# Optimization experiments

Measured on AMD Instinct MI355X. Metric: run time of the kernel, lower is better.

The kernel has to match this reference:

```python
import jax, jax.numpy as jnp
import numpy as np

N_NODES = 50000
N_EDGES = 800000
IN_DIM = 768
HID = 256
OUT = 9
EDGE_FEAT = 100
N_TYPES = 50
N_DIST = 128
P_DROP = 0.4


def _argcn_conv(x, src, dst, etype, edist, W_msg, W_root, b, type_emb, dist_emb, gate_w, gate_b, n_nodes):
    """Edge-type/distance gated relational graph conv.
    x: [N, in]; src/dst/etype/edist: [E]; returns [N, out].
    """
    # per-edge feature from type + distance embeddings -> scalar gate
    ef = jnp.concatenate([type_emb[etype], dist_emb[edist]], axis=-1)  # [E, 2*EDGE_FEAT]
    alpha = jax.nn.sigmoid(ef @ gate_w + gate_b)                       # [E, 1]
    # transform at nodes first (N x in x out GEMM), then gather per edge
    xt = x @ W_msg                                                     # [N, out]
    msg = alpha * xt[src]                                              # [E, out]
    agg = jax.ops.segment_sum(msg, dst, num_segments=n_nodes)         # [N, out]
    return agg + x @ W_root + b


def setup_inputs() -> dict:
    key = jax.random.key(0)
    ks = jax.random.split(key, 20)
    s_in = 1.0 / np.sqrt(IN_DIM)
    s_hid = 1.0 / np.sqrt(HID)
    s_ef = 1.0 / np.sqrt(2 * EDGE_FEAT)
    inp = {
        "x": jax.random.normal(ks[0], (N_NODES, IN_DIM), dtype=jnp.float32),
        "edge_index": jax.random.randint(ks[1], (2, N_EDGES), 0, N_NODES, dtype=jnp.int64 if jax.config.jax_enable_x64 else jnp.int32),
        "edge_type": jax.random.randint(ks[2], (N_EDGES,), 0, N_TYPES, dtype=jnp.int32),
        "edge_distance": jax.random.randint(ks[3], (N_EDGES,), 0, N_DIST, dtype=jnp.int32),
        "drop1": jax.random.uniform(ks[4], (N_NODES, HID), dtype=jnp.float32),
        "drop2": jax.random.uniform(ks[5], (N_NODES, OUT), dtype=jnp.float32),
        # conv1 params
        "W1_msg": jax.random.normal(ks[6], (IN_DIM, HID), dtype=jnp.float32) * s_in,
        "W1_root": jax.random.normal(ks[7], (IN_DIM, HID), dtype=jnp.float32) * s_in,
        "b1": jnp.zeros((HID,), dtype=jnp.float32),
        "te1": jax.random.normal(ks[8], (N_TYPES, EDGE_FEAT), dtype=jnp.float32) * 0.02,
        "de1": jax.random.normal(ks[9], (N_DIST, EDGE_FEAT), dtype=jnp.float32) * 0.02,
        "g1_w": jax.random.normal(ks[10], (2 * EDGE_FEAT, 1), dtype=jnp.float32) * s_ef,
        "g1_b": jnp.zeros((1,), dtype=jnp.float32),
        # conv2 params
        "W2_msg": jax.random.normal(ks[11], (HID, OUT), dtype=jnp.float32) * s_hid,
        "W2_root": jax.random.normal(ks[12], (HID, OUT), dtype=jnp.float32) * s_hid,
        "b2": jnp.zeros((OUT,), dtype=jnp.float32),
        "te2": jax.random.normal(ks[13], (N_TYPES, EDGE_FEAT), dtype=jnp.float32) * 0.02,
        "de2": jax.random.normal(ks[14], (N_DIST, EDGE_FEAT), dtype=jnp.float32) * 0.02,
        "g2_w": jax.random.normal(ks[15], (2 * EDGE_FEAT, 1), dtype=jnp.float32) * s_ef,
        "g2_b": jnp.zeros((1,), dtype=jnp.float32),
    }
    return inp


def reference(x, edge_index, edge_type, edge_distance, drop1, drop2,
              W1_msg, W1_root, b1, te1, de1, g1_w, g1_b,
              W2_msg, W2_root, b2, te2, de2, g2_w, g2_b):
    src, dst = edge_index[0], edge_index[1]
    n = x.shape[0]
    inv_keep = 1.0 / (1.0 - P_DROP)
    m1 = (drop1 >= P_DROP).astype(x.dtype) * inv_keep  # inverted dropout mask
    m2 = (drop2 >= P_DROP).astype(x.dtype) * inv_keep

    h = _argcn_conv(x, src, dst, edge_type, edge_distance,
                    W1_msg, W1_root, b1, te1, de1, g1_w, g1_b, n)
    h = jax.nn.relu(h * m1)
    h = _argcn_conv(h, src, dst, edge_type, edge_distance,
                    W2_msg, W2_root, b2, te2, de2, g2_w, g2_b, n)
    h = jax.nn.relu(h * m2)
    return h
```

## Files before the change

kernel.cpp:

```cpp
#include <hip/hip_runtime.h>
#include <math.h>

#define N_NODES   50000
#define N_EDGESC  800000
#define IN_DIM    768
#define HID       256
#define OUT_DIM   9
#define EDGE_FEAT 100
#define P_DROP    0.4f
#define INV_KEEP  (1.0f/0.6f)

typedef __attribute__((ext_vector_type(8))) short bf16x8;
typedef __attribute__((ext_vector_type(4))) float f32x4;

__device__ __forceinline__ ushort f2bf(float f) {
    uint u = __float_as_uint(f);
    uint r = (u + 0x7fffu + ((u >> 16) & 1u)) >> 16;
    return (ushort)r;
}
__device__ __forceinline__ float bf2f(ushort h) {
    return __uint_as_float(((uint)h) << 16);
}

__device__ __forceinline__ int swz1(int row, int byte) { return byte ^ (((row >> 1) & 3) << 4); }
__device__ __forceinline__ int swz2(int row, int byte) { return byte ^ ((row & 7) << 4); }

__global__ void gate_tables(const float* __restrict__ te1, const float* __restrict__ de1,
                            const float* __restrict__ g1w,
                            const float* __restrict__ te2, const float* __restrict__ de2,
                            const float* __restrict__ g2w,
                            float* __restrict__ tbl) {
    int t = threadIdx.x;
    const float* vec; const float* w;
    if (t < 50)       { vec = te1 + t*EDGE_FEAT;         w = g1w; }
    else if (t < 178) { vec = de1 + (t-50)*EDGE_FEAT;    w = g1w + EDGE_FEAT; }
    else if (t < 228) { vec = te2 + (t-178)*EDGE_FEAT;   w = g2w; }
    else if (t < 356) { vec = de2 + (t-228)*EDGE_FEAT;   w = g2w + EDGE_FEAT; }
    else return;
    float s = 0.f;
    for (int i = 0; i < EDGE_FEAT; ++i) s += vec[i]*w[i];
    tbl[t] = s;
}

__global__ __launch_bounds__(256) void bt_prep(const float* __restrict__ Wm, const float* __restrict__ Wr,
                                               ushort* __restrict__ BTh, ushort* __restrict__ BTl) {
    int tid = blockIdx.x*256 + threadIdx.x;
    if (tid >= 512*IN_DIM) return;
    int n = tid / IN_DIM, k = tid % IN_DIM;
    float w = (n < HID) ? Wm[(size_t)k*HID + n] : Wr[(size_t)k*HID + (n - HID)];
    ushort hi = f2bf(w);
    BTh[tid] = hi;
    BTl[tid] = f2bf(w - bf2f(hi));
}

__global__ __launch_bounds__(256) void w2_pack(const float* __restrict__ Wm, const float* __restrict__ Wr,
                                               ushort* __restrict__ WPT) {
    int i = blockIdx.x*256 + threadIdx.x;
    if (i >= 32*256) return;
    int col = i >> 8, k = i & 255;
    float v = 0.f;
    if (col < 9)                    v = Wm[(size_t)k*OUT_DIM + col];
    else if (col >= 16 && col < 25) v = Wr[(size_t)k*OUT_DIM + (col - 16)];
    WPT[i] = f2bf(v);
}

__global__ __launch_bounds__(256) void zero_deg(int* __restrict__ deg) {
    int i = blockIdx.x*256 + threadIdx.x;
    if (i < N_NODES) deg[i] = 0;
}

__global__ __launch_bounds__(256) void hist(const int* __restrict__ dst, int* __restrict__ deg) {
    int e = blockIdx.x*256 + threadIdx.x;
    if (e < N_EDGESC) atomicAdd(&deg[dst[e]], 1);
}

__global__ __launch_bounds__(256) void scan_p1(const int* __restrict__ deg, int* __restrict__ bsum) {
    __shared__ int sd[256];
    int i = blockIdx.x*256 + threadIdx.x;
    sd[threadIdx.x] = (i < N_NODES) ? deg[i] : 0;
    __syncthreads();
    for (int off = 128; off; off >>= 1) {
        if (threadIdx.x < off) sd[threadIdx.x] += sd[threadIdx.x + off];
        __syncthreads();
    }
    if (!threadIdx.x) bsum[blockIdx.x] = sd[0];
}

__global__ __launch_bounds__(256) void scan_p2(const int* __restrict__ bsum, int* __restrict__ boff) {
    __shared__ int ps[256];
    const int t = threadIdx.x;
    const int NB = 196;
    int v = (t < NB) ? bsum[t] : 0;
    ps[t] = v;
    __syncthreads();
    for (int off = 1; off < 256; off <<= 1) {
        int u = (t >= off) ? ps[t-off] : 0;
        __syncthreads();
        ps[t] += u;
        __syncthreads();
    }
    if (t < NB) boff[t] = ps[t] - v;
}

__global__ __launch_bounds__(256) void scan_p3(const int* __restrict__ deg, const int* __restrict__ boff,
                                               int* __restrict__ rowptr, int* __restrict__ cursor) {
    __shared__ int ps[256];
    const int t = threadIdx.x;
    const int i = blockIdx.x*256 + t;
    int v = (i < N_NODES) ? deg[i] : 0;
    ps[t] = v;
    __syncthreads();
    for (int off = 1; off < 256; off <<= 1) {
        int u = (t >= off) ? ps[t-off] : 0;
        __syncthreads();
        ps[t] += u;
        __syncthreads();
    }
    if (i < N_NODES) {
        int ex = boff[blockIdx.x] + ps[t] - v;
        rowptr[i] = ex;
        cursor[i] = ex;
        if (i == N_NODES-1) rowptr[N_NODES] = ex + v;
    }
}

__global__ __launch_bounds__(256) void fill_csr(const int* __restrict__ src, const int* __restrict__ dst,
                                                const int* __restrict__ etype, const int* __restrict__ edist,
                                                const float* __restrict__ tbl,
                                                const float* __restrict__ g1b, const float* __restrict__ g2b,
                                                int* __restrict__ cursor,
                                                int* __restrict__ esrc, float* __restrict__ a1, float* __restrict__ a2) {
    int e = blockIdx.x*256 + threadIdx.x;
    if (e >= N_EDGESC) return;
    const int tt = etype[e], dd = edist[e];
    const float z1 = tbl[tt]       + tbl[50 + dd]  + g1b[0];
    const float z2 = tbl[178 + tt] + tbl[228 + dd] + g2b[0];
    const int pos = atomicAdd(&cursor[dst[e]], 1);
    esrc[pos] = src[e];
    a1[pos] = 1.f / (1.f + expf(-z1));
    a2[pos] = 1.f / (1.f + expf(-z2));
}

__global__ __launch_bounds__(256) void gemm1_mfma(const float* __restrict__ x,
                                                  const ushort* __restrict__ BTh,
                                                  const ushort* __restrict__ BTl,
                                                  const float* __restrict__ b1,
                                                  ushort* __restrict__ xtb,
                                                  float* __restrict__ h) {
    __shared__ __align__(16) ushort Ah[128*32];
    __shared__ __align__(16) ushort Al[128*32];
    __shared__ __align__(16) ushort Bh[128*32];
    __shared__ __align__(16) ushort Bl[128*32];

    const int t    = threadIdx.x;
    const int wave = t >> 6, lane = t & 63;
    const int wm   = wave >> 1, wn = wave & 1;
    const int nb   = blockIdx.x;
    const int m0   = blockIdx.y * 128;
    const int n0   = nb * 128;

    const int sr = t >> 1;
    const int sk = (t & 1) * 16;
    const int arow   = m0 + sr;
    const bool avalid = arow < N_NODES;
    const float*  ap  = x   + (size_t)(avalid ? arow : 0) * IN_DIM + sk;
    const ushort* bph = BTh + (size_t)(n0 + sr) * IN_DIM + sk;
    const ushort* bpl = BTl + (size_t)(n0 + sr) * IN_DIM + sk;

    const int fr = lane & 15;
    const int kg = lane >> 4;

    f32x4 acc[4][4];
    #pragma unroll
    for (int i=0;i<4;i++)
        #pragma unroll
        for (int j=0;j<4;j++) acc[i][j] = (f32x4){0.f,0.f,0.f,0.f};

    float av[16];
    uint4 bhv0, bhv1, blv0, blv1;
    auto stage_load = [&](int kb) {
        if (avalid) {
            const float4* p = (const float4*)(ap + kb);
            float4 v0 = p[0], v1 = p[1], v2 = p[2], v3 = p[3];
            av[0]=v0.x; av[1]=v0.y; av[2]=v0.z; av[3]=v0.w;
            av[4]=v1.x; av[5]=v1.y; av[6]=v1.z; av[7]=v1.w;
            av[8]=v2.x; av[9]=v2.y; av[10]=v2.z; av[11]=v2.w;
            av[12]=v3.x; av[13]=v3.y; av[14]=v3.z; av[15]=v3.w;
        } else {
            #pragma unroll
            for (int j=0;j<16;j++) av[j]=0.f;
        }
        const uint4* ph = (const uint4*)(bph + kb);
        const uint4* pl = (const uint4*)(bpl + kb);
        bhv0 = ph[0]; bhv1 = ph[1];
        blv0 = pl[0]; blv1 = pl[1];
    };

    char* const cAh = (char*)Ah;
    char* const cAl = (char*)Al;
    char* const cBh = (char*)Bh;
    char* const cBl = (char*)Bl;
    const int wb0 = sr*64 + sk*2;

    stage_load(0);
    for (int kb = 0; kb < IN_DIM; kb += 32) {
        __syncthreads();
        uint hp[8], lp[8];
        #pragma unroll
        for (int jj=0;jj<8;jj++) {
            float v0 = av[2*jj], v1 = av[2*jj+1];
            ushort h0 = f2bf(v0), h1 = f2bf(v1);
            ushort l0 = f2bf(v0 - bf2f(h0)), l1 = f2bf(v1 - bf2f(h1));
            hp[jj] = (uint)h0 | ((uint)h1 << 16);
            lp[jj] = (uint)l0 | ((uint)l1 << 16);
        }
        *(uint4*)(cAh + swz1(sr, wb0))      = *(uint4*)&hp[0];
        *(uint4*)(cAh + swz1(sr, wb0+16))   = *(uint4*)&hp[4];
        *(uint4*)(cAl + swz1(sr, wb0))      = *(uint4*)&lp[0];
        *(uint4*)(cAl + swz1(sr, wb0+16))   = *(uint4*)&lp[4];
        *(uint4*)(cBh + swz1(sr, wb0))      = bhv0;
        *(uint4*)(cBh + swz1(sr, wb0+16))   = bhv1;
        *(uint4*)(cBl + swz1(sr, wb0))      = blv0;
        *(uint4*)(cBl + swz1(sr, wb0+16))   = blv1;
        __syncthreads();
        if (kb + 32 < IN_DIM) stage_load(kb + 32);

        bf16x8 afh[4], afl[4], bfh[4], bfl[4];
        #pragma unroll
        for (int i=0;i<4;i++) {
            const int r = wm*64 + i*16 + fr;
            afh[i] = *(const bf16x8*)(cAh + swz1(r, r*64 + kg*16));
            afl[i] = *(const bf16x8*)(cAl + swz1(r, r*64 + kg*16));
        }
        #pragma unroll
        for (int j=0;j<4;j++) {
            const int c = wn*64 + j*16 + fr;
            bfh[j] = *(const bf16x8*)(cBh + swz1(c, c*64 + kg*16));
            bfl[j] = *(const bf16x8*)(cBl + swz1(c, c*64 + kg*16));
        }
        #pragma unroll
        for (int i=0;i<4;i++)
            #pragma unroll
            for (int j=0;j<4;j++) {
                acc[i][j] = __builtin_amdgcn_mfma_f32_16x16x32_bf16(afh[i], bfh[j], acc[i][j], 0, 0, 0);
                acc[i][j] = __builtin_amdgcn_mfma_f32_16x16x32_bf16(afh[i], bfl[j], acc[i][j], 0, 0, 0);
                acc[i][j] = __builtin_amdgcn_mfma_f32_16x16x32_bf16(afl[i], bfh[j], acc[i][j], 0, 0, 0);
            }
    }

    const bool is_root = (nb >= 2);
    if (is_root) {
        const int cb = n0 - 256;
        #pragma unroll
        for (int j=0;j<4;j++) {
            const int col  = cb + wn*64 + j*16 + fr;
            const float bias = b1[col];
            #pragma unroll
            for (int i=0;i<4;i++) {
                const int rbase = m0 + wm*64 + i*16 + kg*4;
                #pragma unroll
                for (int r=0;r<4;r++) {
                    const int row = rbase + r;
                    if (row < N_NODES) h[(size_t)row*HID + col] = acc[i][j][r] + bias;
                }
            }
        }
    } else {
        #pragma unroll
        for (int j=0;j<4;j++) {
            const int col = n0 + wn*64 + j*16 + fr;
            #pragma unroll
            for (int i=0;i<4;i++) {
                const int rbase = m0 + wm*64 + i*16 + kg*4;
                #pragma unroll
                for (int r=0;r<4;r++) {
                    const int row = rbase + r;
                    if (row < N_NODES) xtb[(size_t)row*HID + col] = f2bf(acc[i][j][r]);
                }
            }
        }
    }
}

__global__ __launch_bounds__(256) void gather1(const int* __restrict__ rowptr,
                                               const int* __restrict__ esrc, const float* __restrict__ a1,
                                               const ushort* __restrict__ xtb,
                                               const float* __restrict__ h,
                                               const float* __restrict__ drop1,
                                               ushort* __restrict__ hb) {
    const int node = blockIdx.x*4 + (threadIdx.x >> 6);
    const int lane = threadIdx.x & 63;
    if (node >= N_NODES) return;
    const int half = lane >> 5, li = lane & 31;
    const int colbase = li*8;
    const int beg = rowptr[node], end = rowptr[node+1];

    float acc[8];
    #pragma unroll
    for (int q=0;q<8;q++) acc[q] = 0.f;

    for (int j = beg; j < end; j += 2) {
        const int jj = j + half;
        int s; float a;
        if (jj < end) { s = esrc[jj]; a = a1[jj]; }
        else          { s = esrc[j];  a = 0.f;    }
        const uint4 v = *(const uint4*)(xtb + (size_t)s*HID + colbase);
        const uint* vw = (const uint*)&v;
        #pragma unroll
        for (int q=0;q<4;q++) {
            acc[2*q]   = fmaf(a, bf2f((ushort)(vw[q] & 0xffffu)), acc[2*q]);
            acc[2*q+1] = fmaf(a, bf2f((ushort)(vw[q] >> 16)),     acc[2*q+1]);
        }
    }
    #pragma unroll
    for (int q=0;q<8;q++) acc[q] += __shfl_xor(acc[q], 32, 64);

    if (half == 0) {
        const float* hp = h + (size_t)node*HID + colbase;
        const float* dp = drop1 + (size_t)node*HID + colbase;
        float hv[8], dv[8];
        *(float4*)&hv[0] = *(const float4*)hp;     *(float4*)&hv[4] = *(const float4*)(hp+4);
        *(float4*)&dv[0] = *(const float4*)dp;     *(float4*)&dv[4] = *(const float4*)(dp+4);
        uint o[4];
        #pragma unroll
        for (int q=0;q<4;q++) {
            float m0 = (dv[2*q]   >= P_DROP) ? INV_KEEP : 0.f;
            float m1 = (dv[2*q+1] >= P_DROP) ? INV_KEEP : 0.f;
            float f0 = fmaxf((hv[2*q]   + acc[2*q])   * m0, 0.f);
            float f1 = fmaxf((hv[2*q+1] + acc[2*q+1]) * m1, 0.f);
            o[q] = (uint)f2bf(f0) | ((uint)f2bf(f1) << 16);
        }
        *(uint4*)(hb + (size_t)node*HID + colbase) = *(uint4*)o;
    }
}

__global__ __launch_bounds__(256) void gemm2_mfma(const ushort* __restrict__ hb,
                                                  const ushort* __restrict__ WPT,
                                                  const float* __restrict__ b2,
                                                  float* __restrict__ ht2, float* __restrict__ root2) {
    __shared__ __align__(16) ushort As[128*256];
    __shared__ __align__(16) ushort Bs[32*256];

    const int t = threadIdx.x;
    const int m0 = blockIdx.x * 128;
    char* const cAs = (char*)As;
    char* const cBs = (char*)Bs;

    #pragma unroll
    for (int i = 0; i < 4; ++i) {
        const int idx = (i*256 + t) * 8;
        const int row = idx >> 8, col = idx & 255;
        const uint4 v = *(const uint4*)(WPT + row*256 + col);
        *(uint4*)(cBs + swz2(row, row*512 + col*2)) = v;
    }
    #pragma unroll
    for (int i = 0; i < 16; ++i) {
        const int idx = (i*256 + t) * 8;
        const int row = idx >> 8, col = idx & 255;
        const int gr = m0 + row;
        uint4 v = make_uint4(0u,0u,0u,0u);
        if (gr < N_NODES) v = *(const uint4*)(hb + (size_t)gr*HID + col);
        *(uint4*)(cAs + swz2(row, row*512 + col*2)) = v;
    }
    __syncthreads();

    const int w = t >> 6, lane = t & 63;
    const int fr = lane & 15, kg = lane >> 4;

    f32x4 acc[2][2];
    #pragma unroll
    for (int i=0;i<2;i++)
        #pragma unroll
        for (int j=0;j<2;j++) acc[i][j] = (f32x4){0.f,0.f,0.f,0.f};

    #pragma unroll
    for (int ks = 0; ks < 8; ++ks) {
        bf16x8 af[2], bfv[2];
        #pragma unroll
        for (int i=0;i<2;i++) {
            const int r = w*32 + i*16 + fr;
            af[i] = *(const bf16x8*)(cAs + swz2(r, r*512 + ks*64 + kg*16));
        }
        #pragma unroll
        for (int j=0;j<2;j++) {
            const int c = j*16 + fr;
            bfv[j] = *(const bf16x8*)(cBs + swz2(c, c*512 + ks*64 + kg*16));
        }
        #pragma unroll
        for (int i=0;i<2;i++)
            #pragma unroll
            for (int j=0;j<2;j++)
                acc[i][j] = __builtin_amdgcn_mfma_f32_16x16x32_bf16(af[i], bfv[j], acc[i][j], 0, 0, 0);
    }

    if (fr < OUT_DIM) {
        const float bias = b2[fr];
        #pragma unroll
        for (int i=0;i<2;i++) {
            const int rbase = m0 + w*32 + i*16 + kg*4;
            #pragma unroll
            for (int r=0;r<4;r++) {
                const int row = rbase + r;
                if (row < N_NODES) {
                    ht2  [(size_t)row*OUT_DIM + fr] = acc[i][0][r];
                    root2[(size_t)row*OUT_DIM + fr] = acc[i][1][r] + bias;
                }
            }
        }
    }
}

__global__ __launch_bounds__(256) void gather2(const int* __restrict__ rowptr,
                                               const int* __restrict__ esrc, const float* __restrict__ a2,
                                               const float* __restrict__ ht2,
                                               const float* __restrict__ root2,
                                               const float* __restrict__ drop2,
                                               float* __restrict__ outp) {
    const int n = blockIdx.x*256 + threadIdx.x;
    if (n >= N_NODES) return;
    float acc[OUT_DIM];
    #pragma unroll
    for (int k=0;k<OUT_DIM;k++) acc[k] = root2[(size_t)n*OUT_DIM + k];
    const int beg = rowptr[n], end = rowptr[n+1];
    for (int j = beg; j < end; ++j) {
        const int s = esrc[j];
        const float a = a2[j];
        const float* sp = ht2 + (size_t)s*OUT_DIM;
        #pragma unroll
        for (int k=0;k<OUT_DIM;k++) acc[k] = fmaf(a, sp[k], acc[k]);
    }
    #pragma unroll
    for (int k=0;k<OUT_DIM;k++) {
        const float m = (drop2[(size_t)n*OUT_DIM + k] >= P_DROP) ? INV_KEEP : 0.f;
        const float v = acc[k]*m;
        outp[(size_t)n*OUT_DIM + k] = v > 0.f ? v : 0.f;
    }
}

extern "C" void kernel_launch(void* const* d_in, const int* in_sizes, int n_in,
                              void* d_out, int out_size, void* d_ws, size_t ws_size,
                              hipStream_t stream) {
    const float* x      = (const float*)d_in[0];
    const int*   eidx   = (const int*)d_in[1];
    const int*   etype  = (const int*)d_in[2];
    const int*   edist  = (const int*)d_in[3];
    const float* drop1  = (const float*)d_in[4];
    const float* drop2  = (const float*)d_in[5];
    const float* W1m    = (const float*)d_in[6];
    const float* W1r    = (const float*)d_in[7];
    const float* b1     = (const float*)d_in[8];
    const float* te1    = (const float*)d_in[9];
    const float* de1    = (const float*)d_in[10];
    const float* g1w    = (const float*)d_in[11];
    const float* g1b    = (const float*)d_in[12];
    const float* W2m    = (const float*)d_in[13];
    const float* W2r    = (const float*)d_in[14];
    const float* b2     = (const float*)d_in[15];
    const float* te2    = (const float*)d_in[16];
    const float* de2    = (const float*)d_in[17];
    const float* g2w    = (const float*)d_in[18];
    const float* g2b    = (const float*)d_in[19];
    float* out = (float*)d_out;

    const int* src = eidx;
    const int* dst = eidx + N_EDGESC;

    float* ws    = (float*)d_ws;
    float* h     = ws;
    float* ht2   = h     + (size_t)N_NODES*HID;
    float* root2 = ht2   + (size_t)N_NODES*OUT_DIM;
    float* tbl   = root2 + (size_t)N_NODES*OUT_DIM;
    float* a1    = tbl   + 384;
    float* a2    = a1    + N_EDGESC;
    int*   esrc  = (int*)(a2 + N_EDGESC);
    int*   deg   = esrc  + N_EDGESC;
    int*   rowptr= deg   + N_NODES;
    int*   cursor= rowptr+ 50004;
    int*   bsum  = cursor+ 50004;
    int*   boff  = bsum  + 256;
    ushort* xtb  = (ushort*)(boff + 256);
    ushort* hb   = xtb + (size_t)N_NODES*HID;
    ushort* BTh  = hb  + (size_t)N_NODES*HID;
    ushort* BTl  = BTh + (size_t)512*IN_DIM;
    ushort* WPT  = BTl + (size_t)512*IN_DIM;

    gate_tables<<<1, 512, 0, stream>>>(te1, de1, g1w, te2, de2, g2w, tbl);
    bt_prep<<<(512*IN_DIM+255)/256, 256, 0, stream>>>(W1m, W1r, BTh, BTl);
    w2_pack<<<32, 256, 0, stream>>>(W2m, W2r, WPT);
    zero_deg<<<(N_NODES+255)/256, 256, 0, stream>>>(deg);
    hist<<<(N_EDGESC+255)/256, 256, 0, stream>>>(dst, deg);
    scan_p1<<<196, 256, 0, stream>>>(deg, bsum);
    scan_p2<<<1, 256, 0, stream>>>(bsum, boff);
    scan_p3<<<196, 256, 0, stream>>>(deg, boff, rowptr, cursor);
    fill_csr<<<(N_EDGESC+255)/256, 256, 0, stream>>>(src, dst, etype, edist, tbl, g1b, g2b,
                                                     cursor, esrc, a1, a2);
    gemm1_mfma<<<dim3(4, (N_NODES+127)/128), 256, 0, stream>>>(x, BTh, BTl, b1, xtb, h);
    gather1<<<(N_NODES+3)/4, 256, 0, stream>>>(rowptr, esrc, a1, xtb, h, drop1, hb);
    gemm2_mfma<<<(N_NODES+127)/128, 256, 0, stream>>>(hb, WPT, b2, ht2, root2);
    gather2<<<(N_NODES+255)/256, 256, 0, stream>>>(rowptr, esrc, a2, ht2, root2, drop2, out);
}
```

Measured before the change: 656.2 us.

## Drop split-bf16 GEMM emulation, widen K tile, and restructure gather1 lanes

The first GEMM stops emulating fp32 with three bf16 MFMAs (hi/lo splits) and uses a single bf16 MFMA per tile, removing the low-part weight buffer and its shared-memory staging. The K tile grows from 32 to 64 with a new swizzle, and the conversion uses a packed bf16x2 intrinsic. The gather1 kernel now processes four edges at a time per wave with 16 columns per lane, reducing across lane groups with two shuffles. This cuts MFMA work and memory traffic roughly threefold in GEMM1, at the cost of lower precision in the first layer's products, which could affect accuracy tolerance.

```diff
diff --git a/kernel.cpp b/kernel.cpp
--- a/kernel.cpp
+++ b/kernel.cpp
@@ -1,4 +1,5 @@
 #include <hip/hip_runtime.h>
+#include <hip/hip_bf16.h>
 #include <math.h>
 
 #define N_NODES   50000
@@ -21,8 +22,11 @@
 __device__ __forceinline__ float bf2f(ushort h) {
     return __uint_as_float(((uint)h) << 16);
 }
-
-__device__ __forceinline__ int swz1(int row, int byte) { return byte ^ (((row >> 1) & 3) << 4); }
+__device__ __forceinline__ uint pack_bf2(float a, float b) {
+    __hip_bfloat162 h2 = __float22bfloat162_rn(make_float2(a, b));
+    uint r; __builtin_memcpy(&r, &h2, 4); return r;
+}
+
 __device__ __forceinline__ int swz2(int row, int byte) { return byte ^ ((row & 7) << 4); }
 
 __global__ void gate_tables(const float* __restrict__ te1, const float* __restrict__ de1,
@@ -43,14 +47,12 @@
 }
 
 __global__ __launch_bounds__(256) void bt_prep(const float* __restrict__ Wm, const float* __restrict__ Wr,
-                                               ushort* __restrict__ BTh, ushort* __restrict__ BTl) {
+                                               ushort* __restrict__ BTh) {
     int tid = blockIdx.x*256 + threadIdx.x;
     if (tid >= 512*IN_DIM) return;
     int n = tid / IN_DIM, k = tid % IN_DIM;
     float w = (n < HID) ? Wm[(size_t)k*HID + n] : Wr[(size_t)k*HID + (n - HID)];
-    ushort hi = f2bf(w);
-    BTh[tid] = hi;
-    BTl[tid] = f2bf(w - bf2f(hi));
+    BTh[tid] = f2bf(w);
 }
 
 __global__ __launch_bounds__(256) void w2_pack(const float* __restrict__ Wm, const float* __restrict__ Wr,
@@ -141,16 +143,15 @@
     a2[pos] = 1.f / (1.f + expf(-z2));
 }
 
+#define G1_BK 64
+
 __global__ __launch_bounds__(256) void gemm1_mfma(const float* __restrict__ x,
                                                   const ushort* __restrict__ BTh,
-                                                  const ushort* __restrict__ BTl,
                                                   const float* __restrict__ b1,
                                                   ushort* __restrict__ xtb,
                                                   float* __restrict__ h) {
-    __shared__ __align__(16) ushort Ah[128*32];
-    __shared__ __align__(16) ushort Al[128*32];
-    __shared__ __align__(16) ushort Bh[128*32];
-    __shared__ __align__(16) ushort Bl[128*32];
+    __shared__ __align__(16) ushort Ah[128*G1_BK];
+    __shared__ __align__(16) ushort Bh[128*G1_BK];
 
     const int t    = threadIdx.x;
     const int wave = t >> 6, lane = t & 63;
@@ -160,12 +161,11 @@
     const int n0   = nb * 128;
 
     const int sr = t >> 1;
-    const int sk = (t & 1) * 16;
+    const int sk = (t & 1) * 32;
     const int arow   = m0 + sr;
     const bool avalid = arow < N_NODES;
-    const float*  ap  = x   + (size_t)(avalid ? arow : 0) * IN_DIM + sk;
-    const ushort* bph = BTh + (size_t)(n0 + sr) * IN_DIM + sk;
-    const ushort* bpl = BTl + (size_t)(n0 + sr) * IN_DIM + sk;
+    const float*  ap = x   + (size_t)(avalid ? arow : 0) * IN_DIM + sk;
+    const ushort* bp = BTh + (size_t)(n0 + sr) * IN_DIM + sk;
 
     const int fr = lane & 15;
     const int kg = lane >> 4;
@@ -176,76 +176,64 @@
         #pragma unroll
         for (int j=0;j<4;j++) acc[i][j] = (f32x4){0.f,0.f,0.f,0.f};
 
-    float av[16];
-    uint4 bhv0, bhv1, blv0, blv1;
+    float4 avf[8]; uint4 bv[4];
     auto stage_load = [&](int kb) {
         if (avalid) {
             const float4* p = (const float4*)(ap + kb);
-            float4 v0 = p[0], v1 = p[1], v2 = p[2], v3 = p[3];
-            av[0]=v0.x; av[1]=v0.y; av[2]=v0.z; av[3]=v0.w;
-            av[4]=v1.x; av[5]=v1.y; av[6]=v1.z; av[7]=v1.w;
-            av[8]=v2.x; av[9]=v2.y; av[10]=v2.z; av[11]=v2.w;
-            av[12]=v3.x; av[13]=v3.y; av[14]=v3.z; av[15]=v3.w;
+            #pragma unroll
+            for (int i=0;i<8;i++) avf[i] = p[i];
         } else {
             #pragma unroll
-            for (int j=0;j<16;j++) av[j]=0.f;
-        }
-        const uint4* ph = (const uint4*)(bph + kb);
-        const uint4* pl = (const uint4*)(bpl + kb);
-        bhv0 = ph[0]; bhv1 = ph[1];
-        blv0 = pl[0]; blv1 = pl[1];
+            for (int i=0;i<8;i++) avf[i] = make_float4(0.f,0.f,0.f,0.f);
+        }
+        const uint4* pb = (const uint4*)(bp + kb);
+        #pragma unroll
+        for (int i=0;i<4;i++) bv[i] = pb[i];
     };
 
-    char* const cAh = (char*)Ah;
-    char* const cAl = (char*)Al;
-    char* const cBh = (char*)Bh;
-    char* const cBl = (char*)Bl;
-    const int wb0 = sr*64 + sk*2;
+    char* const cA = (char*)Ah;
+    char* const cB = (char*)Bh;
+    const int wb = sr*128 + sk*2;
 
     stage_load(0);
-    for (int kb = 0; kb < IN_DIM; kb += 32) {
-        __syncthreads();
-        uint hp[8], lp[8];
-        #pragma unroll
-        for (int jj=0;jj<8;jj++) {
-            float v0 = av[2*jj], v1 = av[2*jj+1];
-            ushort h0 = f2bf(v0), h1 = f2bf(v1);
-            ushort l0 = f2bf(v0 - bf2f(h0)), l1 = f2bf(v1 - bf2f(h1));
-            hp[jj] = (uint)h0 | ((uint)h1 << 16);
-            lp[jj] = (uint)l0 | ((uint)l1 << 16);
-        }
-        *(uint4*)(cAh + swz1(sr, wb0))      = *(uint4*)&hp[0];
-        *(uint4*)(cAh + swz1(sr, wb0+16))   = *(uint4*)&hp[4];
-        *(uint4*)(cAl + swz1(sr, wb0))      = *(uint4*)&lp[0];
-        *(uint4*)(cAl + swz1(sr, wb0+16))   = *(uint4*)&lp[4];
-        *(uint4*)(cBh + swz1(sr, wb0))      = bhv0;
-        *(uint4*)(cBh + swz1(sr, wb0+16))   = bhv1;
-        *(uint4*)(cBl + swz1(sr, wb0))      = blv0;
-        *(uint4*)(cBl + swz1(sr, wb0+16))   = blv1;
-        __syncthreads();
-        if (kb + 32 < IN_DIM) stage_load(kb + 32);
-
-        bf16x8 afh[4], afl[4], bfh[4], bfl[4];
-        #pragma unroll
-        for (int i=0;i<4;i++) {
-            const int r = wm*64 + i*16 + fr;
-            afh[i] = *(const bf16x8*)(cAh + swz1(r, r*64 + kg*16));
-            afl[i] = *(const bf16x8*)(cAl + swz1(r, r*64 + kg*16));
-        }
-        #pragma unroll
-        for (int j=0;j<4;j++) {
-            const int c = wn*64 + j*16 + fr;
-            bfh[j] = *(const bf16x8*)(cBh + swz1(c, c*64 + kg*16));
-            bfl[j] = *(const bf16x8*)(cBl + swz1(c, c*64 + kg*16));
-        }
-        #pragma unroll
-        for (int i=0;i<4;i++)
+    for (int kb = 0; kb < IN_DIM; kb += G1_BK) {
+        __syncthreads();
+        uint au[16];
+        #pragma unroll
+        for (int i=0;i<8;i++) {
+            au[2*i]   = pack_bf2(avf[i].x, avf[i].y);
+            au[2*i+1] = pack_bf2(avf[i].z, avf[i].w);
+        }
+        *(uint4*)(cA + swz2(sr, wb))    = *(uint4*)&au[0];
+        *(uint4*)(cA + swz2(sr, wb+16)) = *(uint4*)&au[4];
+        *(uint4*)(cA + swz2(sr, wb+32)) = *(uint4*)&au[8];
+        *(uint4*)(cA + swz2(sr, wb+48)) = *(uint4*)&au[12];
+        *(uint4*)(cB + swz2(sr, wb))    = bv[0];
+        *(uint4*)(cB + swz2(sr, wb+16)) = bv[1];
+        *(uint4*)(cB + swz2(sr, wb+32)) = bv[2];
+        *(uint4*)(cB + swz2(sr, wb+48)) = bv[3];
+        __syncthreads();
+        if (kb + G1_BK < IN_DIM) stage_load(kb + G1_BK);
+
+        #pragma unroll
+        for (int kk=0; kk<2; kk++) {
+            bf16x8 af[4], bfv[4];
+            #pragma unroll
+            for (int i=0;i<4;i++) {
+                const int r = wm*64 + i*16 + fr;
+                af[i] = *(const bf16x8*)(cA + swz2(r, r*128 + kk*64 + kg*16));
+            }
             #pragma unroll
             for (int j=0;j<4;j++) {
-                acc[i][j] = __builtin_amdgcn_mfma_f32_16x16x32_bf16(afh[i], bfh[j], acc[i][j], 0, 0, 0);
-                acc[i][j] = __builtin_amdgcn_mfma_f32_16x16x32_bf16(afh[i], bfl[j], acc[i][j], 0, 0, 0);
-                acc[i][j] = __builtin_amdgcn_mfma_f32_16x16x32_bf16(afl[i], bfh[j], acc[i][j], 0, 0, 0);
+                const int c = wn*64 + j*16 + fr;
+                bfv[j] = *(const bf16x8*)(cB + swz2(c, c*128 + kk*64 + kg*16));
             }
+            #pragma unroll
+            for (int i=0;i<4;i++)
+                #pragma unroll
+                for (int j=0;j<4;j++)
+                    acc[i][j] = __builtin_amdgcn_mfma_f32_16x16x32_bf16(af[i], bfv[j], acc[i][j], 0, 0, 0);
+        }
     }
 
     const bool is_root = (nb >= 2);
@@ -291,46 +279,58 @@
     const int node = blockIdx.x*4 + (threadIdx.x >> 6);
     const int lane = threadIdx.x & 63;
     if (node >= N_NODES) return;
-    const int half = lane >> 5, li = lane & 31;
-    const int colbase = li*8;
+    const int g = lane >> 4, li = lane & 15;
+    const int colbase = li*16;
     const int beg = rowptr[node], end = rowptr[node+1];
 
-    float acc[8];
-    #pragma unroll
-    for (int q=0;q<8;q++) acc[q] = 0.f;
-
-    for (int j = beg; j < end; j += 2) {
-        const int jj = j + half;
-        int s; float a;
+    float acc[16];
+    #pragma unroll
+    for (int q=0;q<16;q++) acc[q] = 0.f;
+
+    for (int j = beg; j < end; j += 4) {
+        const int jj = j + g;
+        int s = 0; float a = 0.f;
         if (jj < end) { s = esrc[jj]; a = a1[jj]; }
-        else          { s = esrc[j];  a = 0.f;    }
-        const uint4 v = *(const uint4*)(xtb + (size_t)s*HID + colbase);
-        const uint* vw = (const uint*)&v;
+        const ushort* sp = xtb + (size_t)s*HID + colbase;
+        const uint4 v0 = *(const uint4*)sp;
+        const uint4 v1 = *(const uint4*)(sp + 8);
+        const uint* vw0 = (const uint*)&v0;
+        const uint* vw1 = (const uint*)&v1;
         #pragma unroll
         for (int q=0;q<4;q++) {
-            acc[2*q]   = fmaf(a, bf2f((ushort)(vw[q] & 0xffffu)), acc[2*q]);
-            acc[2*q+1] = fmaf(a, bf2f((ushort)(vw[q] >> 16)),     acc[2*q+1]);
-        }
-    }
-    #pragma unroll
-    for (int q=0;q<8;q++) acc[q] += __shfl_xor(acc[q], 32, 64);
-
-    if (half == 0) {
+            acc[2*q]     = fmaf(a, bf2f((ushort)(vw0[q] & 0xffffu)), acc[2*q]);
+            acc[2*q+1]   = fmaf(a, bf2f((ushort)(vw0[q] >> 16)),     acc[2*q+1]);
+            acc[8+2*q]   = fmaf(a, bf2f((ushort)(vw1[q] & 0xffffu)), acc[8+2*q]);
+            acc[8+2*q+1] = fmaf(a, bf2f((ushort)(vw1[q] >> 16)),     acc[8+2*q+1]);
+        }
+    }
+    #pragma unroll
+    for (int q=0;q<16;q++) {
+        acc[q] += __shfl_xor(acc[q], 16, 64);
+        acc[q] += __shfl_xor(acc[q], 32, 64);
+    }
+
+    if (g == 0) {
         const float* hp = h + (size_t)node*HID + colbase;
         const float* dp = drop1 + (size_t)node*HID + colbase;
-        float hv[8], dv[8];
-        *(float4*)&hv[0] = *(const float4*)hp;     *(float4*)&hv[4] = *(const float4*)(hp+4);
-        *(float4*)&dv[0] = *(const float4*)dp;     *(float4*)&dv[4] = *(const float4*)(dp+4);
-        uint o[4];
-        #pragma unroll
-        for (int q=0;q<4;q++) {
+        float hv[16], dv[16];
+        #pragma unroll
+        for (int i=0;i<4;i++) {
+            *(float4*)&hv[4*i] = ((const float4*)hp)[i];
+            *(float4*)&dv[4*i] = ((const float4*)dp)[i];
+        }
+        uint o[8];
+        #pragma unroll
+        for (int q=0;q<8;q++) {
             float m0 = (dv[2*q]   >= P_DROP) ? INV_KEEP : 0.f;
             float m1 = (dv[2*q+1] >= P_DROP) ? INV_KEEP : 0.f;
             float f0 = fmaxf((hv[2*q]   + acc[2*q])   * m0, 0.f);
             float f1 = fmaxf((hv[2*q+1] + acc[2*q+1]) * m1, 0.f);
             o[q] = (uint)f2bf(f0) | ((uint)f2bf(f1) << 16);
         }
-        *(uint4*)(hb + (size_t)node*HID + colbase) = *(uint4*)o;
+        ushort* op = hb + (size_t)node*HID + colbase;
+        *(uint4*)op       = *(uint4*)&o[0];
+        *(uint4*)(op + 8) = *(uint4*)&o[4];
     }
 }
 
@@ -481,11 +481,10 @@
     ushort* xtb  = (ushort*)(boff + 256);
     ushort* hb   = xtb + (size_t)N_NODES*HID;
     ushort* BTh  = hb  + (size_t)N_NODES*HID;
-    ushort* BTl  = BTh + (size_t)512*IN_DIM;
-    ushort* WPT  = BTl + (size_t)512*IN_DIM;
+    ushort* WPT  = BTh + (size_t)512*IN_DIM;
 
     gate_tables<<<1, 512, 0, stream>>>(te1, de1, g1w, te2, de2, g2w, tbl);
-    bt_prep<<<(512*IN_DIM+255)/256, 256, 0, stream>>>(W1m, W1r, BTh, BTl);
+    bt_prep<<<(512*IN_DIM+255)/256, 256, 0, stream>>>(W1m, W1r, BTh);
     w2_pack<<<32, 256, 0, stream>>>(W2m, W2r, WPT);
     zero_deg<<<(N_NODES+255)/256, 256, 0, stream>>>(deg);
     hist<<<(N_EDGESC+255)/256, 256, 0, stream>>>(dst, deg);
@@ -494,7 +493,7 @@
     scan_p3<<<196, 256, 0, stream>>>(deg, boff, rowptr, cursor);
     fill_csr<<<(N_EDGESC+255)/256, 256, 0, stream>>>(src, dst, etype, edist, tbl, g1b, g2b,
                                                      cursor, esrc, a1, a2);
-    gemm1_mfma<<<dim3(4, (N_NODES+127)/128), 256, 0, stream>>>(x, BTh, BTl, b1, xtb, h);
+    gemm1_mfma<<<dim3(4, (N_NODES+127)/128), 256, 0, stream>>>(x, BTh, b1, xtb, h);
     gather1<<<(N_NODES+3)/4, 256, 0, stream>>>(rowptr, esrc, a1, xtb, h, drop1, hb);
     gemm2_mfma<<<(N_NODES+127)/128, 256, 0, stream>>>(hb, WPT, b2, ht2, root2);
     gather2<<<(N_NODES+255)/256, 256, 0, stream>>>(rowptr, esrc, a2, ht2, root2, drop2, out);
```

After: 695.9 us. 1.06x slower.
